# Optimization experiments

Measured on AMD Instinct MI355X. Metric: run time of the kernel, lower is better.

The kernel has to match this reference:

```python
import jax, jax.numpy as jnp
import numpy as np

TOTAL = 131072   # total frames across all utterances
SEG = 256        # number of utterances
FEAT = 78        # input feature dim (hardcoded by Linear(78,1024))
HID = 1024
NCLS = 10


def _linear_params(key, fan_in, fan_out):
    # torch nn.Linear default init: U(-1/sqrt(fan_in), 1/sqrt(fan_in))
    bound = 1.0 / np.sqrt(fan_in)
    kw, kb = jax.random.split(key)
    W = jax.random.uniform(kw, (fan_in, fan_out), minval=-bound, maxval=bound, dtype=jnp.float32)
    b = jax.random.uniform(kb, (fan_out,), minval=-bound, maxval=bound, dtype=jnp.float32)
    return W, b


def setup_inputs() -> dict:
    key = jax.random.key(0)
    ks = jax.random.split(key, 8)
    # ragged lengths summing exactly to TOTAL
    rng = np.random.default_rng(0)
    raw = rng.integers(256, 768, size=SEG).astype(np.float64)
    lens = np.maximum(1, (raw * TOTAL / raw.sum()).astype(np.int64))
    lens[-1] += TOTAL - lens.sum()
    lengths = jnp.asarray(lens, dtype=jnp.int32)

    x = jax.random.normal(ks[0], (TOTAL, FEAT), dtype=jnp.float32)
    W1, b1 = _linear_params(ks[1], FEAT, HID)
    W2, b2 = _linear_params(ks[2], HID, HID)
    W3, b3 = _linear_params(ks[3], HID, HID)
    W4, b4 = _linear_params(ks[4], HID, HID)
    W5, b5 = _linear_params(ks[5], HID, 1)
    W6, b6 = _linear_params(ks[6], HID, HID)
    W7, b7 = _linear_params(ks[7], HID, NCLS)
    return dict(x=x, W1=W1, b1=b1, W2=W2, b2=b2, W3=W3, b3=b3, W4=W4, b4=b4,
                W5=W5, b5=b5, W6=W6, b6=b6, W7=W7, b7=b7, lengths=lengths)


def reference(x, W1, b1, W2, b2, W3, b3, W4, b4, W5, b5, W6, b6, W7, b7, lengths):
    h = jax.nn.relu(x @ W1 + b1)
    h = jax.nn.relu(h @ W2 + b2)
    h = jax.nn.relu(h @ W3 + b3)
    h = jax.nn.relu(h @ W4 + b4)            # [N, HID]
    scores = jax.nn.relu(h @ W5 + b5)[:, 0]  # per-frame attention logit [N]

    # per-segment softmax over frames, then weighted sum pooling (fused segment ops)
    n_seg = lengths.shape[0]
    seg = jnp.repeat(jnp.arange(n_seg, dtype=jnp.int32), lengths,
                     total_repeat_length=h.shape[0])          # [N] segment ids
    m = jax.ops.segment_max(scores, seg, num_segments=n_seg)  # stable softmax max
    e = jnp.exp(scores - m[seg])
    denom = jax.ops.segment_sum(e, seg, num_segments=n_seg)
    w = e / denom[seg]                                        # [N] softmax weights
    pooled = jax.ops.segment_sum(h * w[:, None], seg, num_segments=n_seg)  # [SEG, HID]

    out = jax.nn.relu(pooled @ W6 + b6) @ W7 + b7             # [SEG, 10]
    return out
```

## Files before the change

### kernel.cpp

```cpp
#include <hip/hip_runtime.h>
#include <hip/hip_fp16.h>

#define TOTAL 131072
#define SEGN  256
#define FEAT  78
#define FPAD  96
#define HID   1024
#define NCLS  10
#define FCHUNK 32

typedef __attribute__((ext_vector_type(8))) short short8;
typedef __attribute__((ext_vector_type(4))) float floatx4;

typedef __attribute__((address_space(1))) void gvoid_t;
typedef __attribute__((address_space(3))) void svoid_t;

__device__ __forceinline__ void async_copy16(const void* gsrc, void* ldst) {
    __builtin_amdgcn_global_load_lds((gvoid_t*)(void*)gsrc, (svoid_t*)ldst, 16, 0, 0);
}


__global__ void conv_x_slab(const float* __restrict__ x, __half* __restrict__ xb,
                            int row0, int rows) {
    int idx = blockIdx.x * 256 + threadIdx.x;
    if (idx >= rows * FPAD) return;
    int col = idx % FPAD;
    int r   = idx / FPAD;
    float v = (col < FEAT) ? x[(size_t)(row0 + r) * FEAT + col] : 0.0f;
    xb[idx] = __float2half(v);
}

__global__ void conv_wt_kernel(const float* __restrict__ W, __half* __restrict__ Wt,
                               int K, int N, int Kpad) {
    int idx = blockIdx.x * 256 + threadIdx.x;
    if (idx >= N * Kpad) return;
    int k = idx % Kpad;
    int n = idx / Kpad;
    float v = (k < K) ? W[(size_t)k * N + n] : 0.0f;
    Wt[idx] = __float2half(v);
}

__global__ void conv_w4_kernel(const float* __restrict__ W2, const float* __restrict__ W3,
                               const float* __restrict__ W4, const float* __restrict__ W6,
                               __half* __restrict__ w2t, __half* __restrict__ w3t,
                               __half* __restrict__ w4t, __half* __restrict__ w6t) {
    int idx = blockIdx.x * 256 + threadIdx.x;
    if (idx >= HID * HID) return;
    int k = idx % HID;
    int n = idx / HID;
    const float* Ws[4] = {W2, W3, W4, W6};
    __half* Ts[4] = {w2t, w3t, w4t, w6t};
    int w = blockIdx.y;
    Ts[w][idx] = __float2half(Ws[w][(size_t)k * HID + n]);
}


#define VMCNT(n)  asm volatile("s_waitcnt vmcnt(" #n ")" ::: "memory")
#define SBAR      __builtin_amdgcn_s_barrier()

#define STAGE_A(TT) do { short* d_ = smem + (((TT)&3)<<14); \
    async_copy16(gA + (TT)*32, d_ + t*8); \
    async_copy16(gA + (TT)*32 + kstr128, d_ + 4096 + t*8); } while (0)
#define STAGE_B(TT) do { short* d_ = smem + (((TT)&3)<<14) + 8192; \
    async_copy16(gB + (TT)*32, d_ + t*8); \
    async_copy16(gB + (TT)*32 + kstr128, d_ + 4096 + t*8); } while (0)

#define TILE_BODY(TT, DO_STAGE, VM) do { \
    const short* base_ = smem + (((TT)&3)<<14); \
    short8 af0_[4], af1_[4], bf_[4]; \
    _Pragma("unroll") \
    for (int i_ = 0; i_ < 4; ++i_) af0_[i_] = *(const short8*)&base_[aoff + i_*512]; \
    _Pragma("unroll") \
    for (int i_ = 0; i_ < 4; ++i_) bf_[i_]  = *(const short8*)&base_[8192 + boff + i_*512]; \
    _Pragma("unroll") \
    for (int i_ = 0; i_ < 4; ++i_) af1_[i_] = *(const short8*)&base_[2048 + aoff + i_*512]; \
    if (DO_STAGE) { STAGE_A((TT)+3); STAGE_B((TT)+3); } \
    __builtin_amdgcn_s_setprio(1); \
    _Pragma("unroll") \
    for (int mi_ = 0; mi_ < 4; ++mi_) \
        _Pragma("unroll") \
        for (int ni_ = 0; ni_ < 4; ++ni_) \
            acc[mi_][ni_] = __builtin_amdgcn_mfma_f32_16x16x32_f16( \
                af0_[mi_], bf_[ni_], acc[mi_][ni_], 0, 0, 0); \
    _Pragma("unroll") \
    for (int mi_ = 0; mi_ < 4; ++mi_) \
        _Pragma("unroll") \
        for (int ni_ = 0; ni_ < 4; ++ni_) \
            acc[4+mi_][ni_] = __builtin_amdgcn_mfma_f32_16x16x32_f16( \
                af1_[mi_], bf_[ni_], acc[4+mi_][ni_], 0, 0, 0); \
    __builtin_amdgcn_s_setprio(0); \
    VM; \
    SBAR; \
} while (0)

__global__ __launch_bounds__(512, 2)
void gemm256(const __half* __restrict__ A, const __half* __restrict__ Bt,
             __half* __restrict__ C, const float* __restrict__ bias,
             int M, int N, int K, int relu_flag,
             const float* __restrict__ W5g, float* __restrict__ scores_p)
{
    __shared__ __align__(16) short smem[4 * 16384];

    const int t   = threadIdx.x;
    const int nbn = N >> 8;
    const int nbm = M >> 8;
    int bm, bn;
    {
        const int b = blockIdx.x;
        if ((nbm & 7) == 0) {
            const int xcd = b & 7;
            const int j   = b >> 3;
            bm = xcd * (nbm >> 3) + j / nbn;
            bn = j % nbn;
        } else {
            bn = b % nbn;
            bm = b / nbn;
        }
    }
    const size_t m0 = (size_t)bm << 8;
    const size_t n0 = (size_t)bn << 8;
    const int wave = t >> 6, lane = t & 63;
    const int wmb = (wave >> 2) << 7;
    const int wnb = (wave & 3) << 6;
    const int l16 = lane & 15, q = lane >> 4;
    const int qa  = q ^ ((l16 >> 1) & 3);
    const int aoff = (wmb + l16) * 32 + qa * 8;
    const int boff = (wnb + l16) * 32 + qa * 8;

    const int rr = t >> 2;
    const int qs = ((t & 3) ^ ((t >> 3) & 3)) * 8;
    const __half* gA = A  + (m0 + rr) * K + qs;
    const __half* gB = Bt + (n0 + rr) * K + qs;
    const int kstr128 = K << 7;

    floatx4 acc[8][4] = {};
    const int NT = K >> 5;

    STAGE_A(0); STAGE_B(0);
    STAGE_A(1); STAGE_B(1);
    STAGE_A(2); STAGE_B(2);
    VMCNT(4);
    SBAR;

    int T = 0;
    for (; T < NT - 3; ++T)
        TILE_BODY(T, 1, VMCNT(4));
    TILE_BODY(T, 0, VMCNT(0)); ++T;
    TILE_BODY(T, 0, (void)0);  ++T;
    TILE_BODY(T, 0, (void)0);
    __syncthreads();

    __half* ct = (__half*)smem;
#pragma unroll
    for (int ni = 0; ni < 4; ++ni) {
        const int col = wnb + ni * 16 + l16;
        const float bv = bias[n0 + col];
#pragma unroll
        for (int mi = 0; mi < 8; ++mi) {
            const int r0l = wmb + mi * 16 + q * 4;
#pragma unroll
            for (int r = 0; r < 4; ++r) {
                float v = acc[mi][ni][r] + bv;
                if (relu_flag) v = fmaxf(v, 0.0f);
                ct[(r0l + r) * 256 + col] = __float2half(v);
            }
        }
    }
    __syncthreads();
#pragma unroll
    for (int it = 0; it < 16; ++it) {
        const int chunk = it * 512 + t;
        const int row = chunk >> 5;
        const int c32 = chunk & 31;
        short8 v = *(const short8*)&ct[row * 256 + c32 * 8];
        *(short8*)&C[(m0 + row) * N + n0 + c32 * 8] = v;
        if (scores_p) {
            const float* wv = W5g + n0 + c32 * 8;
            float p = 0.f;
#pragma unroll
            for (int j = 0; j < 8; ++j)
                p += __half2float(((const __half*)&v)[j]) * wv[j];
#pragma unroll
            for (int o = 16; o > 0; o >>= 1) p += __shfl_down(p, o, 32);
            if ((t & 31) == 0)
                scores_p[(size_t)bn * M + m0 + row] = p;
        }
    }
}


__global__ __launch_bounds__(256, 2)
void gemm_f16(const __half* __restrict__ A, const __half* __restrict__ Bt,
              __half* __restrict__ C, const float* __restrict__ bias,
              int M, int N, int K, int relu_flag,
              const float* __restrict__ W5g, float* __restrict__ scores_p)
{
    __shared__ __align__(16) short smem[4 * 128 * 32];
    short* lds_a0 = smem;
    short* lds_a1 = smem + 128 * 32;
    short* lds_b0 = smem + 2 * 128 * 32;
    short* lds_b1 = smem + 3 * 128 * 32;

    const int t   = threadIdx.x;
    const int nbn = N >> 7;
    const int nbm = M >> 7;
    int bm, bn;
    {
        const int b = blockIdx.x;
        if ((nbm & 7) == 0) {
            const int xcd = b & 7;
            const int j   = b >> 3;
            bm = xcd * (nbm >> 3) + j / nbn;
            bn = j % nbn;
        } else {
            bn = b % nbn;
            bm = b / nbn;
        }
    }
    const size_t m0 = (size_t)bm * 128;
    const size_t n0 = (size_t)bn * 128;
    const int wave = t >> 6, lane = t & 63;
    const int wm = (wave >> 1) << 6;
    const int wn = (wave & 1) << 6;
    const int l16 = lane & 15, q = lane >> 4;

    floatx4 acc[4][4] = {};

    const int c0 = t, c1 = t + 256;
    const __half* a0 = A  + (m0 + (size_t)(c0 >> 2)) * K + (c0 & 3) * 8;
    const __half* a1 = A  + (m0 + (size_t)(c1 >> 2)) * K + (c1 & 3) * 8;
    const __half* b0 = Bt + (n0 + (size_t)(c0 >> 2)) * K + (c0 & 3) * 8;
    const __half* b1 = Bt + (n0 + (size_t)(c1 >> 2)) * K + (c1 & 3) * 8;
    short* lA0_0 = &lds_a0[c0 * 8];
    short* lA0_1 = &lds_a0[c1 * 8];
    short* lA1_0 = &lds_a1[c0 * 8];
    short* lA1_1 = &lds_a1[c1 * 8];
    short* lB0_0 = &lds_b0[c0 * 8];
    short* lB0_1 = &lds_b0[c1 * 8];
    short* lB1_0 = &lds_b1[c0 * 8];
    short* lB1_1 = &lds_b1[c1 * 8];

    for (int k0 = 0; k0 < K; k0 += 64) {
        __syncthreads();
        async_copy16(a0 + k0, lA0_0);
        async_copy16(a1 + k0, lA0_1);
        async_copy16(b0 + k0, lB0_0);
        async_copy16(b1 + k0, lB0_1);
        async_copy16(a0 + k0 + 32, lA1_0);
        async_copy16(a1 + k0 + 32, lA1_1);
        async_copy16(b0 + k0 + 32, lB1_0);
        async_copy16(b1 + k0 + 32, lB1_1);
        __syncthreads();

        short8 af[4], bfv[4];
#pragma unroll
        for (int i = 0; i < 4; ++i)
            af[i] = *(const short8*)&lds_a0[(wm + i * 16 + l16) * 32 + q * 8];
#pragma unroll
        for (int i = 0; i < 4; ++i)
            bfv[i] = *(const short8*)&lds_b0[(wn + i * 16 + l16) * 32 + q * 8];
#pragma unroll
        for (int mi = 0; mi < 4; ++mi)
#pragma unroll
            for (int ni = 0; ni < 4; ++ni)
                acc[mi][ni] = __builtin_amdgcn_mfma_f32_16x16x32_f16(
                    af[mi], bfv[ni], acc[mi][ni], 0, 0, 0);

#pragma unroll
        for (int i = 0; i < 4; ++i)
            af[i] = *(const short8*)&lds_a1[(wm + i * 16 + l16) * 32 + q * 8];
#pragma unroll
        for (int i = 0; i < 4; ++i)
            bfv[i] = *(const short8*)&lds_b1[(wn + i * 16 + l16) * 32 + q * 8];
#pragma unroll
        for (int mi = 0; mi < 4; ++mi)
#pragma unroll
            for (int ni = 0; ni < 4; ++ni)
                acc[mi][ni] = __builtin_amdgcn_mfma_f32_16x16x32_f16(
                    af[mi], bfv[ni], acc[mi][ni], 0, 0, 0);
    }

    __half* ct = (__half*)smem;
#pragma unroll
    for (int h = 0; h < 2; ++h) {
        __syncthreads();
        if (wm == h * 64) {
#pragma unroll
            for (int ni = 0; ni < 4; ++ni) {
                const int col = wn + ni * 16 + l16;
                const float bv = bias[n0 + col];
#pragma unroll
                for (int mi = 0; mi < 4; ++mi) {
                    const int r0l = mi * 16 + q * 4;
#pragma unroll
                    for (int r = 0; r < 4; ++r) {
                        float v = acc[mi][ni][r] + bv;
                        if (relu_flag) v = fmaxf(v, 0.0f);
                        ct[(r0l + r) * 128 + col] = __float2half(v);
                    }
                }
            }
        }
        __syncthreads();
#pragma unroll
        for (int it = 0; it < 4; ++it) {
            const int chunk = it * 256 + t;
            const int row = chunk >> 4;
            const int off = (chunk & 15) * 8;
            short8 v = *(const short8*)&ct[row * 128 + off];
            *(short8*)&C[(m0 + h * 64 + row) * N + n0 + off] = v;
            if (scores_p) {
                const float* wv = W5g + n0 + off;
                float p = 0.f;
#pragma unroll
                for (int j = 0; j < 8; ++j)
                    p += __half2float(((const __half*)&v)[j]) * wv[j];
#pragma unroll
                for (int o = 8; o > 0; o >>= 1) p += __shfl_down(p, o, 16);
                if (l16 == 0)
                    scores_p[(size_t)bn * M + m0 + h * 64 + row] = p;
            }
        }
    }
}


__global__ __launch_bounds__(256, 2)
void gemm_k96(const __half* __restrict__ A, const __half* __restrict__ Bt,
              __half* __restrict__ C, const float* __restrict__ bias, int M, int N)
{
    __shared__ __align__(16) short smem[2 * 128 * 96];
    short* lds_a = smem;
    short* lds_b = smem + 128 * 96;

    const int t   = threadIdx.x;
    const int nbn = N >> 7;
    const int nbm = M >> 7;
    int bm, bn;
    {
        const int b = blockIdx.x;
        if ((nbm & 7) == 0) {
            const int xcd = b & 7;
            const int j   = b >> 3;
            bm = xcd * (nbm >> 3) + j / nbn;
            bn = j % nbn;
        } else {
            bn = b % nbn;
            bm = b / nbn;
        }
    }
    const size_t m0 = (size_t)bm * 128;
    const size_t n0 = (size_t)bn * 128;
    const int wave = t >> 6, lane = t & 63;
    const int wm = (wave >> 1) << 6;
    const int wn = (wave & 1) << 6;
    const int l16 = lane & 15, q = lane >> 4;

#pragma unroll
    for (int i = 0; i < 6; ++i) {
        const int c = i * 256 + t;
        const int r = c / 12, j = c % 12;
        async_copy16(A  + (m0 + (size_t)r) * 96 + j * 8, &lds_a[c * 8]);
        async_copy16(Bt + (n0 + (size_t)r) * 96 + j * 8, &lds_b[c * 8]);
    }
    __syncthreads();

    floatx4 acc[4][4] = {};
#pragma unroll
    for (int ks = 0; ks < 3; ++ks) {
        short8 af[4], bfv[4];
        const int xo = ks * 32 + q * 8;
#pragma unroll
        for (int i = 0; i < 4; ++i)
            af[i] = *(const short8*)&lds_a[(wm + i * 16 + l16) * 96 + xo];
#pragma unroll
        for (int i = 0; i < 4; ++i)
            bfv[i] = *(const short8*)&lds_b[(wn + i * 16 + l16) * 96 + xo];
#pragma unroll
        for (int mi = 0; mi < 4; ++mi)
#pragma unroll
            for (int ni = 0; ni < 4; ++ni)
                acc[mi][ni] = __builtin_amdgcn_mfma_f32_16x16x32_f16(
                    af[mi], bfv[ni], acc[mi][ni], 0, 0, 0);
    }

    __half* ct = (__half*)smem;
#pragma unroll
    for (int h = 0; h < 2; ++h) {
        __syncthreads();
        if (wm == h * 64) {
#pragma unroll
            for (int ni = 0; ni < 4; ++ni) {
                const int col = wn + ni * 16 + l16;
                const float bv = bias[n0 + col];
#pragma unroll
                for (int mi = 0; mi < 4; ++mi) {
                    const int r0l = mi * 16 + q * 4;
#pragma unroll
                    for (int r = 0; r < 4; ++r) {
                        float v = fmaxf(acc[mi][ni][r] + bv, 0.0f);
                        ct[(r0l + r) * 128 + col] = __float2half(v);
                    }
                }
            }
        }
        __syncthreads();
#pragma unroll
        for (int it = 0; it < 4; ++it) {
            const int chunk = it * 256 + t;
            const int row = chunk >> 4;
            const int off = (chunk & 15) * 8;
            *(short8*)&C[(m0 + h * 64 + row) * N + n0 + off] =
                *(const short8*)&ct[row * 128 + off];
        }
    }
}


__global__ void seg_offsets_kernel(const int* __restrict__ lengths, int* __restrict__ off) {
    if (blockIdx.x == 0 && threadIdx.x == 0) {
        int a = 0;
        off[0] = 0;
        for (int i = 0; i < SEGN; ++i) { a += lengths[i]; off[i + 1] = a; }
    }
}


__global__ __launch_bounds__(256)
void scorepool_kernel(const __half* __restrict__ h4, int slab_beg, int slab_rows,
                      const float* __restrict__ scores_p, const float* __restrict__ b5,
                      const int* __restrict__ segoff,
                      float* __restrict__ pooled, float* __restrict__ denom)
{
    __shared__ float e_sh[FCHUNK];
    const int t = threadIdx.x;
    const int f0 = slab_beg + blockIdx.x * FCHUNK;

    if (t < FCHUNK) {
        const int fl = f0 - slab_beg + t;
        float sc = 0.f;
#pragma unroll
        for (int b = 0; b < 4; ++b) sc += scores_p[(size_t)b * slab_rows + fl];
        sc = fmaxf(sc + b5[0], 0.0f);
        e_sh[t] = __expf(fminf(sc, 80.0f));
    }
    __syncthreads();

    const int c0 = t * 4;
    int lo = 0, hi = SEGN - 1;
    while (lo < hi) {
        int mid = (lo + hi + 1) >> 1;
        if (segoff[mid] <= f0) lo = mid; else hi = mid - 1;
    }
    int s = lo;
    int f = f0;
    const int fend = f0 + FCHUNK;
    const __half* base = h4 + (size_t)(f0 - slab_beg) * HID + c0;
    while (f < fend) {
        int send = segoff[s + 1];
        if (send > fend) send = fend;
        float a0 = 0.f, a1 = 0.f, a2 = 0.f, a3 = 0.f, es = 0.f;
        for (; f < send; ++f, base += HID) {
            float e = e_sh[f - f0];
            const __half2* r2 = (const __half2*)base;
            float2 u = __half22float2(r2[0]);
            float2 v = __half22float2(r2[1]);
            a0 += e * u.x; a1 += e * u.y; a2 += e * v.x; a3 += e * v.y;
            es += e;
        }
        float* p = pooled + (size_t)s * HID + c0;
        atomicAdd(p,     a0);
        atomicAdd(p + 1, a1);
        atomicAdd(p + 2, a2);
        atomicAdd(p + 3, a3);
        if (t == 0) atomicAdd(&denom[s], es);
        ++s;
    }
}


__global__ __launch_bounds__(256)
void finalize_pool_kernel(const float* __restrict__ pooled, const float* __restrict__ denom,
                          __half* __restrict__ poolh)
{
    int s = blockIdx.x, t = threadIdx.x;
    float inv = 1.0f / denom[s];
    for (int j = t; j < HID; j += 256)
        poolh[(size_t)s * HID + j] = __float2half(pooled[(size_t)s * HID + j] * inv);
}


__global__ void final_kernel(const __half* __restrict__ z, const float* __restrict__ W7,
                             const float* __restrict__ b7, float* __restrict__ out) {
    int s = blockIdx.x, t = threadIdx.x;
    float loc[NCLS];
#pragma unroll
    for (int c = 0; c < NCLS; ++c) loc[c] = 0.f;
    for (int k = t; k < HID; k += 256) {
        float zk = __half2float(z[(size_t)s * HID + k]);
        const float* wr = W7 + k * NCLS;
#pragma unroll
        for (int c = 0; c < NCLS; ++c) loc[c] += zk * wr[c];
    }
#pragma unroll
    for (int c = 0; c < NCLS; ++c)
#pragma unroll
        for (int o = 32; o > 0; o >>= 1) loc[c] += __shfl_down(loc[c], o);
    __shared__ float accs[NCLS];
    if (t < NCLS) accs[t] = 0.f;
    __syncthreads();
    if ((t & 63) == 0)
        for (int c = 0; c < NCLS; ++c) atomicAdd(&accs[c], loc[c]);
    __syncthreads();
    if (t < NCLS) out[s * NCLS + t] = accs[t] + b7[t];
}


extern "C" void kernel_launch(void* const* d_in, const int* in_sizes, int n_in,
                              void* d_out, int out_size, void* d_ws, size_t ws_size,
                              hipStream_t stream) {
    const float* x  = (const float*)d_in[0];
    const float* W1 = (const float*)d_in[1];
    const float* b1 = (const float*)d_in[2];
    const float* W2 = (const float*)d_in[3];
    const float* b2 = (const float*)d_in[4];
    const float* W3 = (const float*)d_in[5];
    const float* b3 = (const float*)d_in[6];
    const float* W4 = (const float*)d_in[7];
    const float* b4 = (const float*)d_in[8];
    const float* W5 = (const float*)d_in[9];
    const float* b5 = (const float*)d_in[10];
    const float* W6 = (const float*)d_in[11];
    const float* b6 = (const float*)d_in[12];
    const float* W7 = (const float*)d_in[13];
    const float* b7 = (const float*)d_in[14];
    const int* lengths = (const int*)d_in[15];
    float* out = (float*)d_out;

    char* ws = (char*)d_ws;
    size_t off = 0;
    auto take = [&](size_t bytes) -> char* {
        char* p = ws + off;
        off = (off + bytes + 255) & ~(size_t)255;
        return p;
    };
    __half* w1t   = (__half*)take((size_t)HID * FPAD * 2);
    __half* w2t   = (__half*)take((size_t)HID * HID * 2);
    __half* w3t   = (__half*)take((size_t)HID * HID * 2);
    __half* w4t   = (__half*)take((size_t)HID * HID * 2);
    __half* w6t   = (__half*)take((size_t)HID * HID * 2);
    int*    segoff = (int*)take((SEGN + 1) * 4);
    float*  pooled = (float*)take((size_t)SEGN * HID * 4);
    float*  denom  = (float*)take(SEGN * 4);
    __half* poolh  = (__half*)take((size_t)SEGN * HID * 2);
    __half* z      = (__half*)take((size_t)SEGN * HID * 2);

    int R = TOTAL;
    while (R > 1024) {
        size_t need = off + (size_t)R * FPAD * 2 + 2 * (size_t)R * HID * 2
                    + (size_t)8 * R * 4 + 4 * 256;
        if (need <= ws_size) break;
        R >>= 1;
    }
    __half* slabX    = (__half*)take((size_t)R * FPAD * 2);
    __half* slabA    = (__half*)take((size_t)R * HID * 2);
    __half* slabB    = (__half*)take((size_t)R * HID * 2);
    float*  scores_p = (float*)take((size_t)8 * R * 4);

    seg_offsets_kernel<<<1, 64, 0, stream>>>(lengths, segoff);
    hipMemsetAsync(pooled, 0, (size_t)SEGN * HID * 4, stream);
    hipMemsetAsync(denom, 0, SEGN * 4, stream);

    conv_wt_kernel<<<(HID * FPAD + 255) / 256, 256, 0, stream>>>(W1, w1t, FEAT, HID, FPAD);
    dim3 gW((HID * HID + 255) / 256, 4);
    conv_w4_kernel<<<gW, 256, 0, stream>>>(W2, W3, W4, W6, w2t, w3t, w4t, w6t);

    const int nBlocksSlab = (R / 128) * (HID / 128);
    const int nBlocks256  = (R / 256) * (HID / 256);
    for (int sb = 0; sb < TOTAL; sb += R) {
        conv_x_slab<<<(R * FPAD + 255) / 256, 256, 0, stream>>>(x, slabX, sb, R);
        gemm_k96<<<nBlocksSlab, 256, 0, stream>>>(slabX, w1t, slabA, b1, R, HID);
        gemm256<<<nBlocks256, 512, 0, stream>>>(slabA, w2t, slabB, b2, R, HID, HID, 1,
                                                nullptr, nullptr);
        gemm256<<<nBlocks256, 512, 0, stream>>>(slabB, w3t, slabA, b3, R, HID, HID, 1,
                                                nullptr, nullptr);
        gemm256<<<nBlocks256, 512, 0, stream>>>(slabA, w4t, slabB, b4, R, HID, HID, 1,
                                                W5, scores_p);
        scorepool_kernel<<<R / FCHUNK, 256, 0, stream>>>(slabB, sb, R, scores_p, b5,
                                                         segoff, pooled, denom);
    }

    finalize_pool_kernel<<<SEGN, 256, 0, stream>>>(pooled, denom, poolh);
    const int nBlocksHead = (SEGN / 128) * (HID / 128);
    gemm_f16<<<nBlocksHead, 256, 0, stream>>>(poolh, w6t, z, b6, SEGN, HID, HID, 1,
                                              nullptr, nullptr);
    final_kernel<<<SEGN, 256, 0, stream>>>(z, W7, b7, out);
}
```

Before: 1.240 ms.

## Split GEMM K-tile into four barrier-synchronized MFMA phases interleaved with loads

Restructures the inner loop of the 256x256 fp16 GEMM so each K-tile is processed in four sub-phases. Each phase loads a subset of A/B fragments from LDS, issues one async global-to-LDS copy and runs 8 MFMAs, with workgroup barriers and lgkmcnt waits between phases. The aim is to interleave LDS reads, global prefetches and matrix-core work across the waves (ping-pong style) rather than bursting all loads and then all MFMAs. It adds many more barriers per tile, which may stall waves if the phases are not balanced. The vmcnt thresholds are adjusted to the finer-grained copies.

```diff
diff --git a/kernel.cpp b/kernel.cpp
--- a/kernel.cpp
+++ b/kernel.cpp
@@ -56,39 +56,53 @@
 
 
 #define VMCNT(n)  asm volatile("s_waitcnt vmcnt(" #n ")" ::: "memory")
+#define LGKM0     do { asm volatile("s_waitcnt lgkmcnt(0)" ::: "memory"); \
+                       __builtin_amdgcn_sched_barrier(0); } while (0)
 #define SBAR      __builtin_amdgcn_s_barrier()
 
-#define STAGE_A(TT) do { short* d_ = smem + (((TT)&3)<<14); \
-    async_copy16(gA + (TT)*32, d_ + t*8); \
-    async_copy16(gA + (TT)*32 + kstr128, d_ + 4096 + t*8); } while (0)
-#define STAGE_B(TT) do { short* d_ = smem + (((TT)&3)<<14) + 8192; \
-    async_copy16(gB + (TT)*32, d_ + t*8); \
-    async_copy16(gB + (TT)*32 + kstr128, d_ + 4096 + t*8); } while (0)
-
-#define TILE_BODY(TT, DO_STAGE, VM) do { \
-    const short* base_ = smem + (((TT)&3)<<14); \
-    short8 af0_[4], af1_[4], bf_[4]; \
-    _Pragma("unroll") \
-    for (int i_ = 0; i_ < 4; ++i_) af0_[i_] = *(const short8*)&base_[aoff + i_*512]; \
-    _Pragma("unroll") \
-    for (int i_ = 0; i_ < 4; ++i_) bf_[i_]  = *(const short8*)&base_[8192 + boff + i_*512]; \
-    _Pragma("unroll") \
-    for (int i_ = 0; i_ < 4; ++i_) af1_[i_] = *(const short8*)&base_[2048 + aoff + i_*512]; \
-    if (DO_STAGE) { STAGE_A((TT)+3); STAGE_B((TT)+3); } \
-    __builtin_amdgcn_s_setprio(1); \
+#define STAGE_A1(TT) async_copy16(gA + (TT)*32,            smem + (((TT)&3)<<14) + t*8)
+#define STAGE_A2(TT) async_copy16(gA + (TT)*32 + kstr128,  smem + (((TT)&3)<<14) + 4096 + t*8)
+#define STAGE_B1(TT) async_copy16(gB + (TT)*32,            smem + (((TT)&3)<<14) + 8192 + t*8)
+#define STAGE_B2(TT) async_copy16(gB + (TT)*32 + kstr128,  smem + (((TT)&3)<<14) + 12288 + t*8)
+
+#define MFMA8(AF, BF, MO, NO) \
     _Pragma("unroll") \
     for (int mi_ = 0; mi_ < 4; ++mi_) \
         _Pragma("unroll") \
-        for (int ni_ = 0; ni_ < 4; ++ni_) \
-            acc[mi_][ni_] = __builtin_amdgcn_mfma_f32_16x16x32_f16( \
-                af0_[mi_], bf_[ni_], acc[mi_][ni_], 0, 0, 0); \
+        for (int ni_ = 0; ni_ < 2; ++ni_) \
+            acc[(MO) + mi_][(NO) + ni_] = __builtin_amdgcn_mfma_f32_16x16x32_f16( \
+                AF[mi_], BF[ni_], acc[(MO) + mi_][(NO) + ni_], 0, 0, 0)
+
+#define SUBTILE(TT, STG, VM) do { \
+    const short* base_ = smem + (((TT)&3)<<14); \
+    short8 af_[4], ag_[4], bfA_[2], bfB_[2]; \
+     \
     _Pragma("unroll") \
-    for (int mi_ = 0; mi_ < 4; ++mi_) \
-        _Pragma("unroll") \
-        for (int ni_ = 0; ni_ < 4; ++ni_) \
-            acc[4+mi_][ni_] = __builtin_amdgcn_mfma_f32_16x16x32_f16( \
-                af1_[mi_], bf_[ni_], acc[4+mi_][ni_], 0, 0, 0); \
-    __builtin_amdgcn_s_setprio(0); \
+    for (int i_ = 0; i_ < 4; ++i_) af_[i_]  = *(const short8*)&base_[aoff + i_*512]; \
+    _Pragma("unroll") \
+    for (int i_ = 0; i_ < 2; ++i_) bfA_[i_] = *(const short8*)&base_[8192 + boff + i_*512]; \
+    if (STG) STAGE_A1((TT)+3); \
+    SBAR; LGKM0; \
+    __builtin_amdgcn_s_setprio(1); MFMA8(af_, bfA_, 0, 0); __builtin_amdgcn_s_setprio(0); \
+    SBAR; \
+     \
+    _Pragma("unroll") \
+    for (int i_ = 0; i_ < 2; ++i_) bfB_[i_] = *(const short8*)&base_[8192 + boff + (2+i_)*512]; \
+    if (STG) STAGE_A2((TT)+3); \
+    SBAR; LGKM0; \
+    __builtin_amdgcn_s_setprio(1); MFMA8(af_, bfB_, 0, 2); __builtin_amdgcn_s_setprio(0); \
+    SBAR; \
+     \
+    _Pragma("unroll") \
+    for (int i_ = 0; i_ < 4; ++i_) ag_[i_] = *(const short8*)&base_[2048 + aoff + i_*512]; \
+    if (STG) STAGE_B1((TT)+3); \
+    SBAR; LGKM0; \
+    __builtin_amdgcn_s_setprio(1); MFMA8(ag_, bfA_, 4, 0); __builtin_amdgcn_s_setprio(0); \
+    SBAR; \
+     \
+    if (STG) STAGE_B2((TT)+3); \
+    SBAR; \
+    __builtin_amdgcn_s_setprio(1); MFMA8(ag_, bfB_, 4, 2); __builtin_amdgcn_s_setprio(0); \
     VM; \
     SBAR; \
 } while (0)
@@ -136,18 +150,18 @@
     floatx4 acc[8][4] = {};
     const int NT = K >> 5;
 
-    STAGE_A(0); STAGE_B(0);
-    STAGE_A(1); STAGE_B(1);
-    STAGE_A(2); STAGE_B(2);
-    VMCNT(4);
+    STAGE_A1(0); STAGE_A2(0); STAGE_B1(0); STAGE_B2(0);
+    STAGE_A1(1); STAGE_A2(1); STAGE_B1(1); STAGE_B2(1);
+    STAGE_A1(2); STAGE_A2(2); STAGE_B1(2); STAGE_B2(2);
+    VMCNT(8);
     SBAR;
 
     int T = 0;
     for (; T < NT - 3; ++T)
-        TILE_BODY(T, 1, VMCNT(4));
-    TILE_BODY(T, 0, VMCNT(0)); ++T;
-    TILE_BODY(T, 0, (void)0);  ++T;
-    TILE_BODY(T, 0, (void)0);
+        SUBTILE(T, 1, VMCNT(8));
+    SUBTILE(T, 0, VMCNT(4)); ++T;
+    SUBTILE(T, 0, VMCNT(0)); ++T;
+    SUBTILE(T, 0, (void)0);
     __syncthreads();
 
     __half* ct = (__half*)smem;
```

New measurement: 1.267 ms. 2.2% more time.

## Use 1024-thread blocks with double-buffered LDS in 256x256 GEMM

Applied to the files above, without the earlier changes.

The 256x256 tile GEMM now runs 16 waves per block, each owning a 64x64 sub-tile instead of 128x64, which halves accumulator registers per wave. The LDS pipeline drops from a 4-stage ring with 3 tiles in flight to a 2-stage double buffer that waits for all loads before each barrier. The epilogue writes the output through LDS in two 128-row halves. The aim is more waves to hide latency, at the cost of a shallower prefetch and a full vmcnt(0) wait plus barrier on every K step.

```diff
diff --git a/kernel.cpp b/kernel.cpp
--- a/kernel.cpp
+++ b/kernel.cpp
@@ -55,51 +55,20 @@
 }
 
 
-#define VMCNT(n)  asm volatile("s_waitcnt vmcnt(" #n ")" ::: "memory")
-#define SBAR      __builtin_amdgcn_s_barrier()
-
-#define STAGE_A(TT) do { short* d_ = smem + (((TT)&3)<<14); \
+#define VMCNT0  asm volatile("s_waitcnt vmcnt(0)" ::: "memory")
+#define SBAR    __builtin_amdgcn_s_barrier()
+
+#define STAGE(TT) do { short* d_ = smem + (((TT)&1)<<14); \
     async_copy16(gA + (TT)*32, d_ + t*8); \
-    async_copy16(gA + (TT)*32 + kstr128, d_ + 4096 + t*8); } while (0)
-#define STAGE_B(TT) do { short* d_ = smem + (((TT)&3)<<14) + 8192; \
-    async_copy16(gB + (TT)*32, d_ + t*8); \
-    async_copy16(gB + (TT)*32 + kstr128, d_ + 4096 + t*8); } while (0)
-
-#define TILE_BODY(TT, DO_STAGE, VM) do { \
-    const short* base_ = smem + (((TT)&3)<<14); \
-    short8 af0_[4], af1_[4], bf_[4]; \
-    _Pragma("unroll") \
-    for (int i_ = 0; i_ < 4; ++i_) af0_[i_] = *(const short8*)&base_[aoff + i_*512]; \
-    _Pragma("unroll") \
-    for (int i_ = 0; i_ < 4; ++i_) bf_[i_]  = *(const short8*)&base_[8192 + boff + i_*512]; \
-    _Pragma("unroll") \
-    for (int i_ = 0; i_ < 4; ++i_) af1_[i_] = *(const short8*)&base_[2048 + aoff + i_*512]; \
-    if (DO_STAGE) { STAGE_A((TT)+3); STAGE_B((TT)+3); } \
-    __builtin_amdgcn_s_setprio(1); \
-    _Pragma("unroll") \
-    for (int mi_ = 0; mi_ < 4; ++mi_) \
-        _Pragma("unroll") \
-        for (int ni_ = 0; ni_ < 4; ++ni_) \
-            acc[mi_][ni_] = __builtin_amdgcn_mfma_f32_16x16x32_f16( \
-                af0_[mi_], bf_[ni_], acc[mi_][ni_], 0, 0, 0); \
-    _Pragma("unroll") \
-    for (int mi_ = 0; mi_ < 4; ++mi_) \
-        _Pragma("unroll") \
-        for (int ni_ = 0; ni_ < 4; ++ni_) \
-            acc[4+mi_][ni_] = __builtin_amdgcn_mfma_f32_16x16x32_f16( \
-                af1_[mi_], bf_[ni_], acc[4+mi_][ni_], 0, 0, 0); \
-    __builtin_amdgcn_s_setprio(0); \
-    VM; \
-    SBAR; \
-} while (0)
-
-__global__ __launch_bounds__(512, 2)
+    async_copy16(gB + (TT)*32, d_ + 8192 + t*8); } while (0)
+
+__global__ __launch_bounds__(1024, 4)
 void gemm256(const __half* __restrict__ A, const __half* __restrict__ Bt,
              __half* __restrict__ C, const float* __restrict__ bias,
              int M, int N, int K, int relu_flag,
              const float* __restrict__ W5g, float* __restrict__ scores_p)
 {
-    __shared__ __align__(16) short smem[4 * 16384];
+    __shared__ __align__(16) short smem[2 * 16384];
 
     const int t   = threadIdx.x;
     const int nbn = N >> 8;
@@ -120,7 +89,7 @@
     const size_t m0 = (size_t)bm << 8;
     const size_t n0 = (size_t)bn << 8;
     const int wave = t >> 6, lane = t & 63;
-    const int wmb = (wave >> 2) << 7;
+    const int wmb = (wave >> 2) << 6;
     const int wnb = (wave & 3) << 6;
     const int l16 = lane & 15, q = lane >> 4;
     const int qa  = q ^ ((l16 >> 1) & 3);
@@ -131,59 +100,76 @@
     const int qs = ((t & 3) ^ ((t >> 3) & 3)) * 8;
     const __half* gA = A  + (m0 + rr) * K + qs;
     const __half* gB = Bt + (n0 + rr) * K + qs;
-    const int kstr128 = K << 7;
-
-    floatx4 acc[8][4] = {};
+
+    floatx4 acc[4][4] = {};
     const int NT = K >> 5;
 
-    STAGE_A(0); STAGE_B(0);
-    STAGE_A(1); STAGE_B(1);
-    STAGE_A(2); STAGE_B(2);
-    VMCNT(4);
+    STAGE(0);
+    VMCNT0;
     SBAR;
 
-    int T = 0;
-    for (; T < NT - 3; ++T)
-        TILE_BODY(T, 1, VMCNT(4));
-    TILE_BODY(T, 0, VMCNT(0)); ++T;
-    TILE_BODY(T, 0, (void)0);  ++T;
-    TILE_BODY(T, 0, (void)0);
-    __syncthreads();
+    for (int T = 0; T < NT; ++T) {
+        const short* base_ = smem + ((T & 1) << 14);
+        short8 af[4], bf[4];
+#pragma unroll
+        for (int i = 0; i < 4; ++i)
+            af[i] = *(const short8*)&base_[aoff + i * 512];
+#pragma unroll
+        for (int i = 0; i < 4; ++i)
+            bf[i] = *(const short8*)&base_[8192 + boff + i * 512];
+        if (T < NT - 1) STAGE(T + 1);
+        __builtin_amdgcn_s_setprio(1);
+#pragma unroll
+        for (int mi = 0; mi < 4; ++mi)
+#pragma unroll
+            for (int ni = 0; ni < 4; ++ni)
+                acc[mi][ni] = __builtin_amdgcn_mfma_f32_16x16x32_f16(
+                    af[mi], bf[ni], acc[mi][ni], 0, 0, 0);
+        __builtin_amdgcn_s_setprio(0);
+        VMCNT0;
+        SBAR;
+    }
 
     __half* ct = (__half*)smem;
 #pragma unroll
-    for (int ni = 0; ni < 4; ++ni) {
-        const int col = wnb + ni * 16 + l16;
-        const float bv = bias[n0 + col];
-#pragma unroll
-        for (int mi = 0; mi < 8; ++mi) {
-            const int r0l = wmb + mi * 16 + q * 4;
-#pragma unroll
-            for (int r = 0; r < 4; ++r) {
-                float v = acc[mi][ni][r] + bv;
-                if (relu_flag) v = fmaxf(v, 0.0f);
-                ct[(r0l + r) * 256 + col] = __float2half(v);
+    for (int h = 0; h < 2; ++h) {
+        __syncthreads();
+        if ((wmb >> 7) == h) {
+            const int rbase = (wmb & 127) + q * 4;
+#pragma unroll
+            for (int ni = 0; ni < 4; ++ni) {
+                const int col = wnb + ni * 16 + l16;
+                const float bv = bias[n0 + col];
+#pragma unroll
+                for (int mi = 0; mi < 4; ++mi) {
+#pragma unroll
+                    for (int r = 0; r < 4; ++r) {
+                        float v = acc[mi][ni][r] + bv;
+                        if (relu_flag) v = fmaxf(v, 0.0f);
+                        ct[(rbase + mi * 16 + r) * 256 + col] = __float2half(v);
+                    }
+                }
             }
         }
-    }
-    __syncthreads();
-#pragma unroll
-    for (int it = 0; it < 16; ++it) {
-        const int chunk = it * 512 + t;
-        const int row = chunk >> 5;
-        const int c32 = chunk & 31;
-        short8 v = *(const short8*)&ct[row * 256 + c32 * 8];
-        *(short8*)&C[(m0 + row) * N + n0 + c32 * 8] = v;
-        if (scores_p) {
-            const float* wv = W5g + n0 + c32 * 8;
-            float p = 0.f;
-#pragma unroll
-            for (int j = 0; j < 8; ++j)
-                p += __half2float(((const __half*)&v)[j]) * wv[j];
-#pragma unroll
-            for (int o = 16; o > 0; o >>= 1) p += __shfl_down(p, o, 32);
-            if ((t & 31) == 0)
-                scores_p[(size_t)bn * M + m0 + row] = p;
+        __syncthreads();
+#pragma unroll
+        for (int it = 0; it < 4; ++it) {
+            const int chunk = it * 1024 + t;
+            const int row = chunk >> 5;
+            const int c32 = chunk & 31;
+            short8 v = *(const short8*)&ct[row * 256 + c32 * 8];
+            *(short8*)&C[(m0 + h * 128 + row) * N + n0 + c32 * 8] = v;
+            if (scores_p) {
+                const float* wv = W5g + n0 + c32 * 8;
+                float p = 0.f;
+#pragma unroll
+                for (int j = 0; j < 8; ++j)
+                    p += __half2float(((const __half*)&v)[j]) * wv[j];
+#pragma unroll
+                for (int o = 16; o > 0; o >>= 1) p += __shfl_down(p, o, 32);
+                if ((t & 31) == 0)
+                    scores_p[(size_t)bn * M + m0 + h * 128 + row] = p;
+            }
         }
     }
 }
@@ -580,12 +566,12 @@
     for (int sb = 0; sb < TOTAL; sb += R) {
         conv_x_slab<<<(R * FPAD + 255) / 256, 256, 0, stream>>>(x, slabX, sb, R);
         gemm_k96<<<nBlocksSlab, 256, 0, stream>>>(slabX, w1t, slabA, b1, R, HID);
-        gemm256<<<nBlocks256, 512, 0, stream>>>(slabA, w2t, slabB, b2, R, HID, HID, 1,
-                                                nullptr, nullptr);
-        gemm256<<<nBlocks256, 512, 0, stream>>>(slabB, w3t, slabA, b3, R, HID, HID, 1,
-                                                nullptr, nullptr);
-        gemm256<<<nBlocks256, 512, 0, stream>>>(slabA, w4t, slabB, b4, R, HID, HID, 1,
-                                                W5, scores_p);
+        gemm256<<<nBlocks256, 1024, 0, stream>>>(slabA, w2t, slabB, b2, R, HID, HID, 1,
+                                                 nullptr, nullptr);
+        gemm256<<<nBlocks256, 1024, 0, stream>>>(slabB, w3t, slabA, b3, R, HID, HID, 1,
+                                                 nullptr, nullptr);
+        gemm256<<<nBlocks256, 1024, 0, stream>>>(slabA, w4t, slabB, b4, R, HID, HID, 1,
+                                                 W5, scores_p);
         scorepool_kernel<<<R / FCHUNK, 256, 0, stream>>>(slabB, sb, R, scores_p, b5,
                                                          segoff, pooled, denom);
     }
```

New measurement: 1.260 ms. No clear change (+1.5%).

## Double-buffer LDS fragment reads in registers to overlap with MFMA

Applied to the files above, without the earlier changes.

Restructures the GEMM main loop so the next K-tile's LDS fragments are read into a second register set while the current tile's MFMAs run. The loop is unrolled by two with ping-pong fragment buffers, and the four async copies per stage are merged into one macro. The goal is to hide LDS read latency behind matrix-core work. In exchange it roughly doubles the fragment registers under a 512x2 launch bound, which risks spills or lower occupancy. The epilogue also assumes an even tile count.

```diff
diff --git a/kernel.cpp b/kernel.cpp
--- a/kernel.cpp
+++ b/kernel.cpp
@@ -58,39 +58,37 @@
 #define VMCNT(n)  asm volatile("s_waitcnt vmcnt(" #n ")" ::: "memory")
 #define SBAR      __builtin_amdgcn_s_barrier()
 
-#define STAGE_A(TT) do { short* d_ = smem + (((TT)&3)<<14); \
-    async_copy16(gA + (TT)*32, d_ + t*8); \
-    async_copy16(gA + (TT)*32 + kstr128, d_ + 4096 + t*8); } while (0)
-#define STAGE_B(TT) do { short* d_ = smem + (((TT)&3)<<14) + 8192; \
-    async_copy16(gB + (TT)*32, d_ + t*8); \
-    async_copy16(gB + (TT)*32 + kstr128, d_ + 4096 + t*8); } while (0)
-
-#define TILE_BODY(TT, DO_STAGE, VM) do { \
+#define STAGE(TT) do { short* d_ = smem + (((TT)&3)<<14); \
+    async_copy16(gA + (TT)*32,           d_ + t*8); \
+    async_copy16(gA + (TT)*32 + kstr128, d_ + 4096 + t*8); \
+    async_copy16(gB + (TT)*32,           d_ + 8192 + t*8); \
+    async_copy16(gB + (TT)*32 + kstr128, d_ + 12288 + t*8); } while (0)
+
+#define READF(S, TT) do { \
     const short* base_ = smem + (((TT)&3)<<14); \
-    short8 af0_[4], af1_[4], bf_[4]; \
     _Pragma("unroll") \
-    for (int i_ = 0; i_ < 4; ++i_) af0_[i_] = *(const short8*)&base_[aoff + i_*512]; \
+    for (int i_ = 0; i_ < 4; ++i_) S##_a0[i_] = *(const short8*)&base_[aoff + i_*512]; \
     _Pragma("unroll") \
-    for (int i_ = 0; i_ < 4; ++i_) bf_[i_]  = *(const short8*)&base_[8192 + boff + i_*512]; \
+    for (int i_ = 0; i_ < 4; ++i_) S##_a1[i_] = *(const short8*)&base_[2048 + aoff + i_*512]; \
     _Pragma("unroll") \
-    for (int i_ = 0; i_ < 4; ++i_) af1_[i_] = *(const short8*)&base_[2048 + aoff + i_*512]; \
-    if (DO_STAGE) { STAGE_A((TT)+3); STAGE_B((TT)+3); } \
+    for (int i_ = 0; i_ < 4; ++i_) S##_b[i_]  = *(const short8*)&base_[8192 + boff + i_*512]; \
+} while (0)
+
+#define MFMA32(S) do { \
     __builtin_amdgcn_s_setprio(1); \
     _Pragma("unroll") \
     for (int mi_ = 0; mi_ < 4; ++mi_) \
         _Pragma("unroll") \
         for (int ni_ = 0; ni_ < 4; ++ni_) \
             acc[mi_][ni_] = __builtin_amdgcn_mfma_f32_16x16x32_f16( \
-                af0_[mi_], bf_[ni_], acc[mi_][ni_], 0, 0, 0); \
+                S##_a0[mi_], S##_b[ni_], acc[mi_][ni_], 0, 0, 0); \
     _Pragma("unroll") \
     for (int mi_ = 0; mi_ < 4; ++mi_) \
         _Pragma("unroll") \
         for (int ni_ = 0; ni_ < 4; ++ni_) \
             acc[4+mi_][ni_] = __builtin_amdgcn_mfma_f32_16x16x32_f16( \
-                af1_[mi_], bf_[ni_], acc[4+mi_][ni_], 0, 0, 0); \
+                S##_a1[mi_], S##_b[ni_], acc[4+mi_][ni_], 0, 0, 0); \
     __builtin_amdgcn_s_setprio(0); \
-    VM; \
-    SBAR; \
 } while (0)
 
 __global__ __launch_bounds__(512, 2)
@@ -134,20 +132,33 @@
     const int kstr128 = K << 7;
 
     floatx4 acc[8][4] = {};
+    short8 f0_a0[4], f0_a1[4], f0_b[4];
+    short8 f1_a0[4], f1_a1[4], f1_b[4];
     const int NT = K >> 5;
 
-    STAGE_A(0); STAGE_B(0);
-    STAGE_A(1); STAGE_B(1);
-    STAGE_A(2); STAGE_B(2);
-    VMCNT(4);
+    STAGE(0); STAGE(1); STAGE(2);
+    VMCNT(8);
     SBAR;
+    READF(f0, 0);
 
     int T = 0;
-    for (; T < NT - 3; ++T)
-        TILE_BODY(T, 1, VMCNT(4));
-    TILE_BODY(T, 0, VMCNT(0)); ++T;
-    TILE_BODY(T, 0, (void)0);  ++T;
-    TILE_BODY(T, 0, (void)0);
+    for (; T < NT - 3; T += 2) {
+        VMCNT(4);
+        SBAR;
+        READF(f1, T + 1);
+        STAGE(T + 3);
+        MFMA32(f0);
+        VMCNT(4);
+        SBAR;
+        READF(f0, T + 2);
+        if (T + 4 < NT) STAGE(T + 4);
+        MFMA32(f1);
+    }
+    VMCNT(0);
+    SBAR;
+    READF(f1, NT - 1);
+    MFMA32(f0);
+    MFMA32(f1);
     __syncthreads();
 
     __half* ct = (__half*)smem;
```

Result: no change. 1.222 ms (median of 2 runs) (-1.4%).
